# Optimization experiments

Measured on AMD Instinct MI355X. Metric: run time of the kernel, lower is better.

The kernel has to match this reference:

```python
import jax, jax.numpy as jnp
import numpy as np

BN_EPS = 1e-6


def _conv1x1(x, w, b):
    # x: (B, Cin, N, K), w: (Cout, Cin), b: (Cout,)
    return jnp.einsum('oc,bcnk->bonk', w, x) + b[None, :, None, None]


def _bn(x, gamma, beta, mean, var):
    # inference-mode BatchNorm2d over channel axis 1
    inv = gamma / jnp.sqrt(var + BN_EPS)
    return x * inv[None, :, None, None] + (beta - mean * inv)[None, :, None, None]


def setup_inputs() -> dict:
    key = jax.random.key(0)
    ks = jax.random.split(key, 12)
    B, N, K = 4, 16384, 16
    C_out = 32
    C_img = 2 * C_out - 10          # 54, so concat has 2*C_out = 64 channels
    C_in1 = 2 * C_out               # 64
    C_in2 = 2 * (C_out + 3)         # 70

    points = jax.random.normal(ks[0], (B, N, 3), jnp.float32)
    image_features = jax.random.normal(ks[1], (B, C_img, N, K), jnp.float32)
    dist = jax.random.uniform(ks[2], (B, N, K), jnp.float32)
    idx = jax.random.randint(ks[3], (B, N, K), 0, N, dtype=jnp.int32)

    w1 = jax.random.normal(ks[4], (C_out, C_in1), jnp.float32) / np.sqrt(C_in1).astype(np.float32)
    b1 = jnp.zeros((C_out,), jnp.float32)
    gamma1 = jnp.ones((C_out,), jnp.float32)
    beta1 = jnp.zeros((C_out,), jnp.float32)
    mean1 = 0.1 * jax.random.normal(ks[5], (C_out,), jnp.float32)
    var1 = 0.5 + jax.random.uniform(ks[6], (C_out,), jnp.float32)

    w2 = jax.random.normal(ks[7], (C_out, C_in2), jnp.float32) / np.sqrt(C_in2).astype(np.float32)
    b2 = jnp.zeros((C_out,), jnp.float32)
    gamma2 = jnp.ones((C_out,), jnp.float32)
    beta2 = jnp.zeros((C_out,), jnp.float32)
    mean2 = 0.1 * jax.random.normal(ks[8], (C_out,), jnp.float32)
    var2 = 0.5 + jax.random.uniform(ks[9], (C_out,), jnp.float32)

    return {
        'points': points, 'image_features': image_features, 'dist': dist, 'idx': idx,
        'w1': w1, 'b1': b1, 'gamma1': gamma1, 'beta1': beta1, 'mean1': mean1, 'var1': var1,
        'w2': w2, 'b2': b2, 'gamma2': gamma2, 'beta2': beta2, 'mean2': mean2, 'var2': var2,
    }


def reference(points, image_features, dist, idx,
              w1, b1, gamma1, beta1, mean1, var1,
              w2, b2, gamma2, beta2, mean2, var2):
    B, N, K = idx.shape
    pts = jnp.swapaxes(points, 1, 2)                       # (B, 3, N)
    ep = jnp.broadcast_to(pts[:, :, :, None], (B, 3, N, K))  # extended points
    # KNN gather: nb[b, c, n, k] = pts[b, c, idx[b, n, k]]
    nb = jax.vmap(lambda p, i: p[:, i])(pts, idx)          # (B, 3, N, K)

    concat = jnp.concatenate(
        [ep, nb, ep - nb, dist[:, None, :, :], image_features], axis=1)  # (B, 64, N, K)

    h = jax.nn.relu(_bn(_conv1x1(concat, w1, b1), gamma1, beta1, mean1, var1))  # (B, 32, N, K)
    feat = jnp.concatenate([h, ep], axis=1)                # (B, 35, N, K)

    pooled = jnp.concatenate(
        [jnp.max(feat, axis=-1, keepdims=True),
         jnp.mean(feat, axis=-1, keepdims=True)], axis=1)  # (B, 70, N, 1)

    out = jax.nn.relu(_bn(_conv1x1(pooled, w2, b2), gamma2, beta2, mean2, var2))  # (B, 32, N, 1)
    return out
```

## Files before the change

### kernel.cpp

```cpp
#include <hip/hip_runtime.h>
#include <hip/hip_bf16.h>
#include <cmath>

#define BN_EPS 1e-6f
typedef unsigned int u32;
typedef __attribute__((ext_vector_type(8))) short short8;
typedef __attribute__((ext_vector_type(4))) float f32x4;

constexpr int B_    = 4;
constexpr int N_    = 16384;
constexpr int K_    = 16;
constexpr int C_IMG = 54;
constexpr int C1    = 64;
constexpr int CO    = 32;
constexpr int C2    = 70;
constexpr int NT    = 16;
constexpr int POS   = 256;
constexpr int XSTR  = 34;
constexpr int PPAD  = 76;
constexpr int NK    = N_ * K_;
constexpr int CHUNK = 6;

__device__ inline u32 pkbf(float a, float b) {
    union { __hip_bfloat162 h; u32 u; } cv;
    cv.h = __float22bfloat162_rn(make_float2(a, b));
    return cv.u;
}

__global__ __launch_bounds__(256, 4) void pif_mfma_kernel(
    const float* __restrict__ points, const float* __restrict__ imgf,
    const float* __restrict__ dist,   const int*   __restrict__ idx,
    const float* __restrict__ w1, const float* __restrict__ b1,
    const float* __restrict__ g1, const float* __restrict__ be1,
    const float* __restrict__ m1, const float* __restrict__ v1,
    const float* __restrict__ w2, const float* __restrict__ b2,
    const float* __restrict__ g2, const float* __restrict__ be2,
    const float* __restrict__ m2, const float* __restrict__ v2,
    float* __restrict__ out)
{
    __shared__ u32   x_lds[POS * XSTR];
    __shared__ float pooled[NT][PPAD];

    const int t   = threadIdx.x;
    const int tpb = N_ / NT;
    const int b   = blockIdx.x / tpb;
    const int n0  = (blockIdx.x % tpb) * NT;
    const int k   = t & 15, ln = t >> 4, n = n0 + ln;

    const int   base_nk = (b * N_ + n) * K_ + k;
    const int   j  = idx[base_nk];
    const float dv = dist[base_nk];
    const int   pb = (b * N_ + n) * 3;
    const float px = points[pb], py = points[pb + 1], pz = points[pb + 2];
    const int   qb = (b * N_ + j) * 3;
    const float qx = points[qb], qy = points[qb + 1], qz = points[qb + 2];

    u32* row = &x_lds[t * XSTR];
    row[0] = pkbf(px, py);
    row[1] = pkbf(pz, qx);
    row[2] = pkbf(qy, qz);
    row[3] = pkbf(px - qx, py - qy);
    row[4] = pkbf(pz - qz, dv);

    const float* ip = imgf + (size_t)b * C_IMG * NK + (n * K_ + k);
    #pragma unroll
    for (int c0 = 0; c0 < C_IMG; c0 += CHUNK) {
        float xv[CHUNK];
        #pragma unroll
        for (int jj = 0; jj < CHUNK; ++jj) xv[jj] = ip[(c0 + jj) * NK];
        row[5 + c0 / 2    ] = pkbf(xv[0], xv[1]);
        row[5 + c0 / 2 + 1] = pkbf(xv[2], xv[3]);
        row[5 + c0 / 2 + 2] = pkbf(xv[4], xv[5]);
    }

    const int w = t >> 6, lane = t & 63, m16 = lane & 15, quad = lane >> 4;

    short8 bfrag[2][2];
    float  inv1v[2], add1v[2];
    #pragma unroll
    for (int ot = 0; ot < 2; ++ot) {
        const int o = ot * 16 + m16;
        #pragma unroll
        for (int kc = 0; kc < 2; ++kc) {
            const float* wr = w1 + o * C1 + kc * 32 + quad * 8;
            union { u32 u[4]; short8 v; } bf;
            bf.u[0] = pkbf(wr[0], wr[1]); bf.u[1] = pkbf(wr[2], wr[3]);
            bf.u[2] = pkbf(wr[4], wr[5]); bf.u[3] = pkbf(wr[6], wr[7]);
            bfrag[ot][kc] = bf.v;
        }
        const float iv = g1[o] * rsqrtf(v1[o] + BN_EPS);
        inv1v[ot] = iv;
        add1v[ot] = be1[o] - m1[o] * iv + b1[o] * iv;
    }

    if (t < 48) {
        const int nn = t & 15, jj = t >> 4;
        const float v = points[(b * N_ + n0 + nn) * 3 + jj];
        pooled[nn][32 + jj] = v;
        pooled[nn][67 + jj] = v;
    }

    __syncthreads();

    f32x4 acc[4][2];
    #pragma unroll
    for (int mt = 0; mt < 4; ++mt)
        #pragma unroll
        for (int ot = 0; ot < 2; ++ot)
            acc[mt][ot] = (f32x4){0.f, 0.f, 0.f, 0.f};

    #pragma unroll
    for (int mt = 0; mt < 4; ++mt) {
        #pragma unroll
        for (int kc = 0; kc < 2; ++kc) {
            const u32* r2 = &x_lds[(w * 64 + mt * 16 + m16) * XSTR + kc * 16 + quad * 4];
            uint2 a0 = *(const uint2*)r2;
            uint2 a1 = *(const uint2*)(r2 + 2);
            union { u32 u[4]; short8 v; } af;
            af.u[0] = a0.x; af.u[1] = a0.y; af.u[2] = a1.x; af.u[3] = a1.y;
            acc[mt][0] = __builtin_amdgcn_mfma_f32_16x16x32_bf16(af.v, bfrag[0][kc], acc[mt][0], 0, 0, 0);
            acc[mt][1] = __builtin_amdgcn_mfma_f32_16x16x32_bf16(af.v, bfrag[1][kc], acc[mt][1], 0, 0, 0);
        }
    }

    #pragma unroll
    for (int mt = 0; mt < 4; ++mt) {
        #pragma unroll
        for (int ot = 0; ot < 2; ++ot) {
            float mx = 0.f, sm = 0.f;
            #pragma unroll
            for (int r = 0; r < 4; ++r) {
                float hv = fmaf(acc[mt][ot][r], inv1v[ot], add1v[ot]);
                hv = fmaxf(hv, 0.f);
                mx = fmaxf(mx, hv);
                sm += hv;
            }
            mx = fmaxf(mx, __shfl_xor(mx, 16));
            mx = fmaxf(mx, __shfl_xor(mx, 32));
            sm += __shfl_xor(sm, 16);
            sm += __shfl_xor(sm, 32);
            if (quad == 0) {
                const int nn = w * 4 + mt;
                pooled[nn][ot * 16 + m16]      = mx;
                pooled[nn][35 + ot * 16 + m16] = sm * (1.f / 16.f);
            }
        }
    }
    __syncthreads();

    #pragma unroll
    for (int r = 0; r < 2; ++r) {
        const int nn = t & 15;
        const int o  = (t >> 4) + r * 16;
        const float* wr = w2 + o * C2;
        float a0 = 0.f, a1 = 0.f;
        #pragma unroll
        for (int c = 0; c < C2; c += 2) {
            a0 = fmaf(wr[c],     pooled[nn][c],     a0);
            a1 = fmaf(wr[c + 1], pooled[nn][c + 1], a1);
        }
        const float acc2 = a0 + a1;
        const float iv = g2[o] * rsqrtf(v2[o] + BN_EPS);
        float ov = fmaf(acc2 + b2[o], iv, be2[o] - m2[o] * iv);
        ov = fmaxf(ov, 0.f);
        out[(b * CO + o) * N_ + n0 + nn] = ov;
    }
}

extern "C" void kernel_launch(void* const* d_in, const int* in_sizes, int n_in,
                              void* d_out, int out_size, void* d_ws, size_t ws_size,
                              hipStream_t stream) {
    const float* points = (const float*)d_in[0];
    const float* imgf   = (const float*)d_in[1];
    const float* dist   = (const float*)d_in[2];
    const int*   idx    = (const int*)  d_in[3];
    const float* w1     = (const float*)d_in[4];
    const float* b1     = (const float*)d_in[5];
    const float* g1     = (const float*)d_in[6];
    const float* be1    = (const float*)d_in[7];
    const float* m1     = (const float*)d_in[8];
    const float* v1     = (const float*)d_in[9];
    const float* w2     = (const float*)d_in[10];
    const float* b2     = (const float*)d_in[11];
    const float* g2     = (const float*)d_in[12];
    const float* be2    = (const float*)d_in[13];
    const float* m2     = (const float*)d_in[14];
    const float* v2     = (const float*)d_in[15];
    float* out          = (float*)d_out;

    const int blocks = B_ * (N_ / NT);
    pif_mfma_kernel<<<blocks, 256, 0, stream>>>(
        points, imgf, dist, idx,
        w1, b1, g1, be1, m1, v1,
        w2, b2, g2, be2, m2, v2, out);
}
```

Baseline: 356.3 us.

## Vectorize image-feature loads, swizzle LDS rows, and move second conv to MFMA

Image features are now loaded as float4 per thread, each covering four consecutive k positions, and transposed into the LDS activation tile. A XOR swizzle is applied to LDS column addresses to reduce bank conflicts for both the writes and the MFMA fragment reads. The second 1x1 conv is moved from scalar FMA loops to bf16 MFMA with BN folded into the weights, and the pooled input is split into hi/lo bf16 parts to keep precision. This adds an extra barrier and leaves half the waves idle in the final stage.

```diff
diff --git a/kernel.cpp b/kernel.cpp
--- a/kernel.cpp
+++ b/kernel.cpp
@@ -18,14 +18,18 @@
 constexpr int POS   = 256;
 constexpr int XSTR  = 34;
 constexpr int PPAD  = 76;
+constexpr int PBSTR = 50;
 constexpr int NK    = N_ * K_;
-constexpr int CHUNK = 6;
 
 __device__ inline u32 pkbf(float a, float b) {
     union { __hip_bfloat162 h; u32 u; } cv;
     cv.h = __float22bfloat162_rn(make_float2(a, b));
     return cv.u;
 }
+__device__ inline float bf2f(unsigned short s) {
+    union { u32 u; float f; } cv; cv.u = ((u32)s) << 16; return cv.f;
+}
+__device__ inline int SW(int pos) { return ((pos >> 4) & 7) << 2; }
 
 __global__ __launch_bounds__(256, 4) void pif_mfma_kernel(
     const float* __restrict__ points, const float* __restrict__ imgf,
@@ -46,6 +50,7 @@
     const int b   = blockIdx.x / tpb;
     const int n0  = (blockIdx.x % tpb) * NT;
     const int k   = t & 15, ln = t >> 4, n = n0 + ln;
+    const int w = t >> 6, lane = t & 63, m16 = lane & 15, quad = lane >> 4;
 
     const int   base_nk = (b * N_ + n) * K_ + k;
     const int   j  = idx[base_nk];
@@ -55,25 +60,35 @@
     const int   qb = (b * N_ + j) * 3;
     const float qx = points[qb], qy = points[qb + 1], qz = points[qb + 2];
 
-    u32* row = &x_lds[t * XSTR];
-    row[0] = pkbf(px, py);
-    row[1] = pkbf(pz, qx);
-    row[2] = pkbf(qy, qz);
-    row[3] = pkbf(px - qx, py - qy);
-    row[4] = pkbf(pz - qz, dv);
-
-    const float* ip = imgf + (size_t)b * C_IMG * NK + (n * K_ + k);
-    #pragma unroll
-    for (int c0 = 0; c0 < C_IMG; c0 += CHUNK) {
-        float xv[CHUNK];
-        #pragma unroll
-        for (int jj = 0; jj < CHUNK; ++jj) xv[jj] = ip[(c0 + jj) * NK];
-        row[5 + c0 / 2    ] = pkbf(xv[0], xv[1]);
-        row[5 + c0 / 2 + 1] = pkbf(xv[2], xv[3]);
-        row[5 + c0 / 2 + 2] = pkbf(xv[4], xv[5]);
-    }
-
-    const int w = t >> 6, lane = t & 63, m16 = lane & 15, quad = lane >> 4;
+    {
+        u32* row = &x_lds[t * XSTR];
+        const int s = SW(t);
+        row[0 ^ s] = pkbf(px, py);
+        row[1 ^ s] = pkbf(pz, qx);
+        row[2 ^ s] = pkbf(qy, qz);
+        row[3 ^ s] = pkbf(px - qx, py - qy);
+        row[4 ^ s] = pkbf(pz - qz, dv);
+    }
+
+    {
+        const int nn = (t >> 2) & 15, q = t & 3;
+        const int swn = ((nn & 7) << 2);
+        const float* bbase = imgf + (size_t)b * C_IMG * NK + (n0 + nn) * K_ + 4 * q;
+        #pragma unroll
+        for (int it = 0; it < 7; ++it) {
+            const int pp = w + 4 * it;
+            if (pp < 27) {
+                const float4 L0 = *(const float4*)(bbase + (size_t)(2 * pp)     * NK);
+                const float4 L1 = *(const float4*)(bbase + (size_t)(2 * pp + 1) * NK);
+                const int col = (5 + pp) ^ swn;
+                u32* r0 = &x_lds[(nn * 16 + 4 * q) * XSTR + col];
+                r0[0 * XSTR] = pkbf(L0.x, L1.x);
+                r0[1 * XSTR] = pkbf(L0.y, L1.y);
+                r0[2 * XSTR] = pkbf(L0.z, L1.z);
+                r0[3 * XSTR] = pkbf(L0.w, L1.w);
+            }
+        }
+    }
 
     short8 bfrag[2][2];
     float  inv1v[2], add1v[2];
@@ -93,6 +108,27 @@
         add1v[ot] = be1[o] - m1[o] * iv + b1[o] * iv;
     }
 
+    short8 w2frag[3];
+    float  add2 = 0.f;
+    if (w < 2) {
+        const int o = w * 16 + m16;
+        const float iv2 = g2[o] * rsqrtf(v2[o] + BN_EPS);
+        add2 = be2[o] - m2[o] * iv2 + b2[o] * iv2;
+        #pragma unroll
+        for (int kc = 0; kc < 3; ++kc) {
+            float wv[8];
+            #pragma unroll
+            for (int jj = 0; jj < 8; ++jj) {
+                const int c = kc * 32 + quad * 8 + jj;
+                wv[jj] = (c < C2) ? iv2 * w2[o * C2 + c] : 0.f;
+            }
+            union { u32 u[4]; short8 v; } bf;
+            bf.u[0] = pkbf(wv[0], wv[1]); bf.u[1] = pkbf(wv[2], wv[3]);
+            bf.u[2] = pkbf(wv[4], wv[5]); bf.u[3] = pkbf(wv[6], wv[7]);
+            w2frag[kc] = bf.v;
+        }
+    }
+
     if (t < 48) {
         const int nn = t & 15, jj = t >> 4;
         const float v = points[(b * N_ + n0 + nn) * 3 + jj];
@@ -111,9 +147,12 @@
 
     #pragma unroll
     for (int mt = 0; mt < 4; ++mt) {
+        const int posr = w * 64 + mt * 16 + m16;
+        const int s    = ((w * 4 + mt) & 7) << 2;
         #pragma unroll
         for (int kc = 0; kc < 2; ++kc) {
-            const u32* r2 = &x_lds[(w * 64 + mt * 16 + m16) * XSTR + kc * 16 + quad * 4];
+            const int colb = (kc * 16 + quad * 4) ^ s;
+            const u32* r2 = &x_lds[posr * XSTR + colb];
             uint2 a0 = *(const uint2*)r2;
             uint2 a1 = *(const uint2*)(r2 + 2);
             union { u32 u[4]; short8 v; } af;
@@ -148,22 +187,46 @@
     }
     __syncthreads();
 
-    #pragma unroll
-    for (int r = 0; r < 2; ++r) {
-        const int nn = t & 15;
-        const int o  = (t >> 4) + r * 16;
-        const float* wr = w2 + o * C2;
-        float a0 = 0.f, a1 = 0.f;
-        #pragma unroll
-        for (int c = 0; c < C2; c += 2) {
-            a0 = fmaf(wr[c],     pooled[nn][c],     a0);
-            a1 = fmaf(wr[c + 1], pooled[nn][c + 1], a1);
-        }
-        const float acc2 = a0 + a1;
-        const float iv = g2[o] * rsqrtf(v2[o] + BN_EPS);
-        float ov = fmaf(acc2 + b2[o], iv, be2[o] - m2[o] * iv);
-        ov = fmaxf(ov, 0.f);
-        out[(b * CO + o) * N_ + n0 + nn] = ov;
+    u32* pbf_hi = &x_lds[0];
+    u32* pbf_lo = &x_lds[NT * PBSTR];
+    {
+        const int nn = t >> 4, j0 = t & 15;
+        #pragma unroll
+        for (int r = 0; r < 3; ++r) {
+            const int jj = j0 + 16 * r;
+            const int c0 = 2 * jj, c1 = 2 * jj + 1;
+            const float v0 = (c0 < C2) ? pooled[nn][c0] : 0.f;
+            const float v1_ = (c1 < C2) ? pooled[nn][c1] : 0.f;
+            const u32 hi = pkbf(v0, v1_);
+            const float r0 = v0 - bf2f((unsigned short)(hi & 0xffff));
+            const float r1 = v1_ - bf2f((unsigned short)(hi >> 16));
+            pbf_hi[nn * PBSTR + jj] = hi;
+            pbf_lo[nn * PBSTR + jj] = pkbf(r0, r1);
+        }
+    }
+    __syncthreads();
+
+    if (w < 2) {
+        f32x4 d = (f32x4){0.f, 0.f, 0.f, 0.f};
+        #pragma unroll
+        for (int half = 0; half < 2; ++half) {
+            const u32* pb_ = half ? pbf_lo : pbf_hi;
+            #pragma unroll
+            for (int kc = 0; kc < 3; ++kc) {
+                const u32* r2 = &pb_[m16 * PBSTR + kc * 16 + quad * 4];
+                uint2 a0 = *(const uint2*)r2;
+                uint2 a1 = *(const uint2*)(r2 + 2);
+                union { u32 u[4]; short8 v; } af;
+                af.u[0] = a0.x; af.u[1] = a0.y; af.u[2] = a1.x; af.u[3] = a1.y;
+                d = __builtin_amdgcn_mfma_f32_16x16x32_bf16(af.v, w2frag[kc], d, 0, 0, 0);
+            }
+        }
+        const int o = w * 16 + m16;
+        f32x4 ov;
+        #pragma unroll
+        for (int r = 0; r < 4; ++r) ov[r] = fmaxf(d[r] + add2, 0.f);
+        float4* dst = (float4*)&out[(size_t)(b * CO + o) * N_ + n0 + quad * 4];
+        *dst = make_float4(ov[0], ov[1], ov[2], ov[3]);
     }
 }
 
```

After: 356.9 us. About the same (+0.2%).
